# Optimization experiments

Measured on AMD Instinct MI355X. Metric: run time of the kernel, lower is better.

The kernel has to match this reference:

```python
import jax, jax.numpy as jnp
import numpy as np

T, D_ENC, H, D_EMB, VOCAB = 4000, 1024, 1024, 512, 8192
V = VOCAB + 1  # + blank
P = 800
TEMPERATURE = 1.0


def setup_inputs() -> dict:
    key = jax.random.key(0)
    ks = jax.random.split(key, 8)
    s = lambda d: 1.0 / np.sqrt(d)
    return {
        'enc_out': jax.random.normal(ks[0], (T, D_ENC), jnp.float32),
        'embedding': jax.random.normal(ks[1], (V, D_EMB), jnp.float32) * s(D_EMB),
        'W_ih': jax.random.normal(ks[2], (4 * H, D_EMB), jnp.float32) * s(D_EMB),
        'W_hh': jax.random.normal(ks[3], (4 * H, H), jnp.float32) * s(H),
        'b_lstm': jnp.zeros((4 * H,), jnp.float32),
        'W_pred': jax.random.normal(ks[4], (D_ENC, H), jnp.float32) * s(H),
        'b_pred': jnp.zeros((D_ENC,), jnp.float32),
        'W_join': jax.random.normal(ks[5], (V, D_ENC), jnp.float32) * s(D_ENC),
        'b_join': jnp.zeros((V,), jnp.float32),
        'phonemes': jax.random.randint(ks[6], (P,), 0, VOCAB, jnp.int32),
    }


def reference(enc_out, embedding, W_ih, W_hh, b_lstm, W_pred, b_pred, W_join, b_join, phonemes):
    blank_idx = embedding.shape[0] - 1
    n_phon = phonemes.shape[0]

    def predict_step(tok, h, c):
        # one-token RNNT predictor: embed -> LSTM cell -> projection to joiner dim
        x = embedding[tok]
        gates = x @ W_ih.T + h @ W_hh.T + b_lstm  # [4H]
        i, f, g, o = jnp.split(gates, 4)
        i, f, o = jax.nn.sigmoid(i), jax.nn.sigmoid(f), jax.nn.sigmoid(o)
        c2 = f * c + i * jnp.tanh(g)
        h2 = o * jnp.tanh(c2)
        pred = h2 @ W_pred.T + b_pred  # [D_ENC]
        return pred, h2, c2

    def step(carry, enc_t):
        tok, h, c, tp = carry
        pred, h2, c2 = predict_step(tok, h, c)
        logits = (jax.nn.relu(enc_t + pred) @ W_join.T + b_join) / TEMPERATURE
        logp = jax.nn.log_softmax(logits)  # [V]
        pick = jnp.argmax(logp)
        phon_done = tp >= n_phon
        is_blank = (pick == blank_idx) | phon_done
        next_phon = phonemes[jnp.minimum(tp, n_phon - 1)]
        prediction = jnp.where(is_blank, blank_idx, next_phon)
        # blank: keep hypothesis token/state; non-blank: advance to phoneme + new state
        tok2 = jnp.where(is_blank, tok, next_phon)
        h3 = jnp.where(is_blank, h, h2)
        c3 = jnp.where(is_blank, c, c2)
        tp2 = tp + jnp.where(is_blank, 0, 1)
        return (tok2, h3, c3, tp2), (logp, prediction, ~phon_done)

    # initial predictor pass with blank token from zero state (mirrors the warm-up predict call)
    h0 = jnp.zeros((W_hh.shape[1],), enc_out.dtype)
    c0 = jnp.zeros_like(h0)
    _, h_init, c_init = predict_step(jnp.int32(blank_idx), h0, c0)
    carry0 = (jnp.int32(blank_idx), h_init, c_init, jnp.int32(0))
    _, (alignment, predictions, valid) = jax.lax.scan(step, carry0, enc_out)
    return alignment, predictions, valid
```

## Files before the change

kernel.cpp:

```cpp
#include <hip/hip_runtime.h>
#include <math.h>

#define TT     4000
#define DENC   1024
#define HD     1024
#define DEMB   512
#define VD     8193
#define NPH    800
#define BLANK  8192
#define NWG    256
#define NTHR   512
#define CHUNK_M 800
#define NSTEP  (NPH + 2)
#define NSTEPP 802
#define NVT    65
#define NP     129
#define CHUNK  256

typedef __bf16 bf16x4 __attribute__((ext_vector_type(4)));
typedef __bf16 bf16x8 __attribute__((ext_vector_type(8)));
typedef float  f32x16 __attribute__((ext_vector_type(16)));

#define WSF_HHIST  1024
#define WSF_PREDS  822272
#define WSF_HX     1642496
#define WSF_GXT    2053120
#define WSF_PMAX   1642496
#define WSF_PSUM   2158496
#define WSF_PARG   2674496
#define WSF_LSE    3190496
#define WSF_AMAX   3194496
#define WSF_XBF    3195520
#define WSF_W16    4899456
#define WSF_END    9159296
#define NEED_MFMA  ((size_t)36653568)
#define TST_IDX    512
#define HX_BYTE_OFF  ((size_t)WSF_HX * 4)
#define HX_BYTES     ((size_t)NSTEPP * 256 * 8)

#define L_HX     1024
#define L_HHIST  5120
#define L_PREDS  826368
#define F_PMAX 1646592
#define F_PSUM 1906592
#define F_PARG 2166592
#define F_LSE  2426592

#define GEMM_SMEM  12800
#define CHAIN_SMEM (4096 + 64 + 16 * NSTEPP * 2)
#define JOIN_SMEM  (65536 + 128)
#define S_XH   0
#define S_GS   3072
#define S_C4   3088
#define S_TOK  3264
#define S_RED  4066
#define S_AMAX 4082
#define SMEM_FLOATS_F32 4352
#define SMEM_BYTES_F32 (SMEM_FLOATS_F32 * 4)


__device__ __forceinline__ float dot4(float4 a, float4 b, float acc) {
  acc = fmaf(a.x, b.x, acc); acc = fmaf(a.y, b.y, acc);
  acc = fmaf(a.z, b.z, acc); acc = fmaf(a.w, b.w, acc);
  return acc;
}
__device__ __forceinline__ float sigmf(float x) { return 1.f / (1.f + expf(-x)); }
__device__ __forceinline__ float sigm_fast(float x) { return 1.f / (1.f + __expf(-x)); }
__device__ __forceinline__ float tanh_fast(float x) {
  float e = __expf(2.f * x);
  return 1.f - 2.f / (e + 1.f);
}
__device__ __forceinline__ float bfbits_to_f32(unsigned u16v) {
  return __builtin_bit_cast(float, (u16v & 0xFFFFu) << 16);
}

__device__ __forceinline__ void combine3(float& m, float& s, int& am,
                                         float om, float os, int oa) {
  float mm = fmaxf(m, om);
  s = s * __expf(m - mm) + os * __expf(om - mm);
  if (om > m || (om == m && oa < am)) am = oa;
  m = mm;
}

__device__ __forceinline__ void gload16(const void* g, void* l) {
  __builtin_amdgcn_global_load_lds(
      (const __attribute__((address_space(1))) unsigned int*)g,
      (__attribute__((address_space(3))) unsigned int*)l, 16, 0, 0);
}

__device__ __forceinline__ float ld_coh(const float* p) {
  return __hip_atomic_load((const float*)p, __ATOMIC_RELAXED, __HIP_MEMORY_SCOPE_AGENT);
}

__device__ __forceinline__ void light_barrier(unsigned* flags, unsigned& ep) {
  unsigned* arrive  = flags;
  unsigned* release = flags + 256;
  __builtin_amdgcn_s_waitcnt(0);
  __syncthreads();
  if (blockIdx.x == 0) {
    int tid = threadIdx.x;
    if (tid > 0 && tid < NWG) {
      while (__hip_atomic_load(&arrive[tid], __ATOMIC_RELAXED, __HIP_MEMORY_SCOPE_AGENT) != ep) {}
    }
    __syncthreads();
    if (tid == 0)
      __hip_atomic_store(release, ep, __ATOMIC_RELAXED, __HIP_MEMORY_SCOPE_AGENT);
  } else {
    if (threadIdx.x == 0) {
      __hip_atomic_store(&arrive[blockIdx.x], ep, __ATOMIC_RELAXED, __HIP_MEMORY_SCOPE_AGENT);
      while (__hip_atomic_load(release, __ATOMIC_RELAXED, __HIP_MEMORY_SCOPE_AGENT) != ep) {}
    }
    __syncthreads();
  }
  asm volatile("" ::: "memory");
  ep++;
}

__device__ __forceinline__ void heavy_barrier(unsigned* flags) {
  unsigned* bar = flags + 257;
  __syncthreads();
  if (threadIdx.x == 0) {
    __threadfence();
    unsigned g = __hip_atomic_load(&bar[1], __ATOMIC_RELAXED, __HIP_MEMORY_SCOPE_AGENT);
    unsigned v = __hip_atomic_fetch_add(&bar[0], 1u, __ATOMIC_RELAXED, __HIP_MEMORY_SCOPE_AGENT);
    if (v == (unsigned)(NWG - 1)) {
      __hip_atomic_store(&bar[0], 0u, __ATOMIC_RELAXED, __HIP_MEMORY_SCOPE_AGENT);
      __hip_atomic_store(&bar[1], g + 1u, __ATOMIC_RELEASE, __HIP_MEMORY_SCOPE_AGENT);
    } else {
      while (__hip_atomic_load(&bar[1], __ATOMIC_RELAXED, __HIP_MEMORY_SCOPE_AGENT) == g)
        __builtin_amdgcn_s_sleep(1);
    }
    __threadfence();
  }
  __syncthreads();
}

__device__ void xbf_fill(const float* enc, const float* preds, __bf16* dst,
                         int t0, int K, int pi0, int g0, int gs) {
  int total = K << 8;
  for (int q = g0; q < total; q += gs) {
    int j = q >> 8, seg = q & 255;
    int pi = (pi0 < 0) ? NPH : pi0 + j;
    float4 e = ((const float4*)(enc + (size_t)(t0 + j) * 1024))[seg];
    float4 p = ((const float4*)(preds + (size_t)pi * 1024))[seg];
    bf16x4 r;
    r[0] = (__bf16)fmaxf(e.x + p.x, 0.f);
    r[1] = (__bf16)fmaxf(e.y + p.y, 0.f);
    r[2] = (__bf16)fmaxf(e.z + p.z, 0.f);
    r[3] = (__bf16)fmaxf(e.w + p.w, 0.f);
    *(bf16x4*)(dst + (size_t)j * 1024 + (seg << 2)) = r;
  }
}

__device__ void joiner_tiles(const __bf16* W16, const __bf16* xrows, const float* bj,
                             float* out_align, float* pmax, float* psum, int* parg,
                             char* smc, int t0, int K, int tile0, int tstride) {
  const int tid = threadIdx.x;
  const int wid = tid >> 6, lane = tid & 63;
  const int wj = wid & 3, wv = wid >> 2;
  const int l31 = lane & 31, lhi = lane >> 5;
  const int jt_n = (K + 127) >> 7;
  const int ntiles = jt_n * NVT;

  for (int tile = tile0; tile < ntiles; tile += tstride) {
    const int vt = tile % NVT, jt = tile / NVT;
    const int v0 = vt << 7, j0 = jt << 7;
    f32x16 acc0, acc1;
    #pragma unroll
    for (int i = 0; i < 16; ++i) { acc0[i] = 0.f; acc1[i] = 0.f; }

    auto stage = [&](int db, int kb) {
      char* wb = smc + db * 32768;
      char* xb = wb + 16384;
      #pragma unroll
      for (int p = 0; p < 2; ++p) {
        int sbase = p * 512 + wid * 64;
        int s = sbase + lane;
        int ks = s >> 7, r = s & 127;
        gload16(W16 + (size_t)(v0 + r) * 1024 + kb + ks * 8, wb + sbase * 16);
        gload16(xrows + (size_t)(j0 + r) * 1024 + kb + ks * 8, xb + sbase * 16);
      }
    };

    stage(0, 0);
    __syncthreads();
    int db = 0;
    for (int kb16 = 0; kb16 < 16; ++kb16) {
      if (kb16 < 15) stage(db ^ 1, (kb16 + 1) << 6);
      const char* wb = smc + db * 32768;
      const char* xb = wb + 16384;
      #pragma unroll
      for (int k16 = 0; k16 < 4; ++k16) {
        int ks = k16 * 2 + lhi;
        bf16x8 a  = *(const bf16x8*)(xb + ((ks << 7) + (wj << 5) + l31) * 16);
        bf16x8 b0 = *(const bf16x8*)(wb + ((ks << 7) + (wv << 6) + l31) * 16);
        bf16x8 b1 = *(const bf16x8*)(wb + ((ks << 7) + (wv << 6) + 32 + l31) * 16);
        acc0 = __builtin_amdgcn_mfma_f32_32x32x16_bf16(a, b0, acc0, 0, 0, 0);
        acc1 = __builtin_amdgcn_mfma_f32_32x32x16_bf16(a, b1, acc1, 0, 0, 0);
      }
      __syncthreads();
      db ^= 1;
    }

    const int v_0 = v0 + (wv << 6) + l31;
    const int v_1 = v_0 + 32;
    const float bj0 = (v_0 < VD) ? bj[v_0] : 0.f;
    const float bj1 = (v_1 < VD) ? bj[v_1] : 0.f;
    const int jbase = j0 + (wj << 5) + 4 * lhi;
    const bool npok = (v0 + (wv << 6)) < VD;
    const int np = (v0 >> 6) + wv;
    #pragma unroll
    for (int reg = 0; reg < 16; ++reg) {
      int j = jbase + (reg & 3) + 8 * (reg >> 2);
      bool jok = j < K;
      float lg0 = acc0[reg] + bj0;
      float lg1 = acc1[reg] + bj1;
      if (jok) {
        size_t ro = (size_t)(t0 + j) * VD;
        if (v_0 < VD) out_align[ro + v_0] = lg0;
        if (v_1 < VD) out_align[ro + v_1] = lg1;
      }
      float l0 = (v_0 < VD) ? lg0 : -1e30f;
      float l1 = (v_1 < VD) ? lg1 : -1e30f;
      float m = fmaxf(l0, l1);
      float ss = 0.f;
      if (v_0 < VD) ss += __expf(l0 - m);
      if (v_1 < VD) ss += __expf(l1 - m);
      int am = (l1 > l0) ? v_1 : v_0;
      #pragma unroll
      for (int msk = 1; msk <= 16; msk <<= 1) {
        float om = __shfl_xor(m, msk, 64);
        float os = __shfl_xor(ss, msk, 64);
        int oa = __shfl_xor(am, msk, 64);
        float mm = fmaxf(m, om);
        ss = ss * __expf(m - mm) + os * __expf(om - mm);
        if (om > m || (om == m && oa < am)) am = oa;
        m = mm;
      }
      if (l31 == 0 && jok && npok) {
        size_t pb = (size_t)(t0 + j) * NP + np;
        __hip_atomic_store(&pmax[pb], m, __ATOMIC_RELAXED, __HIP_MEMORY_SCOPE_AGENT);
        __hip_atomic_store(&psum[pb], ss, __ATOMIC_RELAXED, __HIP_MEMORY_SCOPE_AGENT);
        __hip_atomic_store(&parg[pb], am, __ATOMIC_RELAXED, __HIP_MEMORY_SCOPE_AGENT);
      }
    }
  }
}

__device__ __forceinline__ void merge_row129(const float* pmax, const float* psum,
                                             const int* parg, int row, int lane,
                                             float& m, float& s, int& am) {
  size_t b = (size_t)row * NP;
  m = ld_coh(pmax + b + lane);
  s = ld_coh(psum + b + lane);
  am = __hip_atomic_load(&parg[b + lane], __ATOMIC_RELAXED, __HIP_MEMORY_SCOPE_AGENT);
  {
    int i2 = lane + 64;
    float om = ld_coh(pmax + b + i2);
    float os = ld_coh(psum + b + i2);
    int oa = __hip_atomic_load(&parg[b + i2], __ATOMIC_RELAXED, __HIP_MEMORY_SCOPE_AGENT);
    combine3(m, s, am, om, os, oa);
  }
  if (lane == 0) {
    float om = ld_coh(pmax + b + 128);
    float os = ld_coh(psum + b + 128);
    int oa = __hip_atomic_load(&parg[b + 128], __ATOMIC_RELAXED, __HIP_MEMORY_SCOPE_AGENT);
    combine3(m, s, am, om, os, oa);
  }
  #pragma unroll
  for (int msk = 32; msk; msk >>= 1) {
    float om = __shfl_xor(m, msk, 64);
    float os = __shfl_xor(s, msk, 64);
    int oa = __shfl_xor(am, msk, 64);
    combine3(m, s, am, om, os, oa);
  }
}

__global__ __launch_bounds__(512) void wconv_kernel(const float* __restrict__ Wjoin,
                                                    float* wsf) {
  __bf16* w16 = (__bf16*)(wsf + WSF_W16);
  int g0 = blockIdx.x * 512 + threadIdx.x;
  int gs = gridDim.x * 512;
  for (int q = g0; q < VD * 256; q += gs) {
    int v = q >> 8, seg = q & 255;
    float4 w4 = ((const float4*)(Wjoin + (size_t)v * 1024))[seg];
    bf16x4 r;
    r[0] = (__bf16)w4.x; r[1] = (__bf16)w4.y; r[2] = (__bf16)w4.z; r[3] = (__bf16)w4.w;
    *(bf16x4*)(w16 + (size_t)v * 1024 + (seg << 2)) = r;
  }
}

__global__ __launch_bounds__(512) void gx_kernel(
    const float* __restrict__ Wih, const float* __restrict__ emb,
    const float* __restrict__ bl, const int* __restrict__ phon, float* wsf) {
  extern __shared__ float sm[];
  float* Wt = sm;
  float* Xt = sm + 2112;
  __bf16* gxT = (__bf16*)(wsf + WSF_GXT);
  const int tid = threadIdx.x;
  const int tx = tid & 31, ty = tid >> 5;
  int ntiles = 32 * 13;
  for (int tile = blockIdx.x; tile < ntiles; tile += gridDim.x) {
    int vt = tile & 31, jt = tile >> 5;
    int v0 = vt * 128, j0 = jt * 64;
    float acc[4][4];
    #pragma unroll
    for (int a = 0; a < 4; ++a)
      #pragma unroll
      for (int q = 0; q < 4; ++q) acc[a][q] = 0.f;
    for (int kk = 0; kk < DEMB; kk += 16) {
      {
        int r = tid >> 2, seg = tid & 3;
        float4 wv = ((const float4*)(Wih + (size_t)(v0 + r) * DEMB + kk))[seg];
        Wt[(seg * 4 + 0) * 132 + r] = wv.x;
        Wt[(seg * 4 + 1) * 132 + r] = wv.y;
        Wt[(seg * 4 + 2) * 132 + r] = wv.z;
        Wt[(seg * 4 + 3) * 132 + r] = wv.w;
      }
      if (tid < 256) {
        int r = tid >> 2, seg = tid & 3;
        int j = j0 + r;
        float4 xv = make_float4(0.f, 0.f, 0.f, 0.f);
        if (j < NSTEP) {
          int tok = (j < 2) ? BLANK : phon[j - 2];
          xv = ((const float4*)(emb + (size_t)tok * DEMB + kk))[seg];
        }
        Xt[(seg * 4 + 0) * 68 + r] = xv.x;
        Xt[(seg * 4 + 1) * 68 + r] = xv.y;
        Xt[(seg * 4 + 2) * 68 + r] = xv.z;
        Xt[(seg * 4 + 3) * 68 + r] = xv.w;
      }
      __syncthreads();
      #pragma unroll
      for (int k = 0; k < 16; ++k) {
        float4 a = *(const float4*)(Wt + k * 132 + (tx << 2));
        float4 bq = *(const float4*)(Xt + k * 68 + (ty << 2));
        acc[0][0] = fmaf(a.x, bq.x, acc[0][0]); acc[1][0] = fmaf(a.y, bq.x, acc[1][0]);
        acc[2][0] = fmaf(a.z, bq.x, acc[2][0]); acc[3][0] = fmaf(a.w, bq.x, acc[3][0]);
        acc[0][1] = fmaf(a.x, bq.y, acc[0][1]); acc[1][1] = fmaf(a.y, bq.y, acc[1][1]);
        acc[2][1] = fmaf(a.z, bq.y, acc[2][1]); acc[3][1] = fmaf(a.w, bq.y, acc[3][1]);
        acc[0][2] = fmaf(a.x, bq.z, acc[0][2]); acc[1][2] = fmaf(a.y, bq.z, acc[1][2]);
        acc[2][2] = fmaf(a.z, bq.z, acc[2][2]); acc[3][2] = fmaf(a.w, bq.z, acc[3][2]);
        acc[0][3] = fmaf(a.x, bq.w, acc[0][3]); acc[1][3] = fmaf(a.y, bq.w, acc[1][3]);
        acc[2][3] = fmaf(a.z, bq.w, acc[2][3]); acc[3][3] = fmaf(a.w, bq.w, acc[3][3]);
      }
      __syncthreads();
    }
    int vb = v0 + (tx << 2), jb0 = j0 + (ty << 2);
    #pragma unroll
    for (int jj = 0; jj < 4; ++jj) {
      int j = jb0 + jj;
      if (j >= NSTEP) continue;
      #pragma unroll
      for (int q = 0; q < 4; ++q)
        gxT[(size_t)(vb + q) * NSTEPP + j] = (__bf16)(acc[q][jj] + bl[vb + q]);
    }
  }
}

__global__ __launch_bounds__(NTHR) void chain_kernel(const float* __restrict__ Whh,
                                                     float* wsf) {
  extern __shared__ float sm[];
  float* hcur = sm;
  float* GS = sm + 1024;
  __bf16* gxl = (__bf16*)(sm + 1024 + 16);
  const int tid = threadIdx.x;
  const int w = tid >> 6, l = tid & 63;
  const int b = blockIdx.x;
  const __bf16* gxT = (const __bf16*)(wsf + WSF_GXT);
  float* hhist = wsf + WSF_HHIST;
  unsigned long long* hx = (unsigned long long*)(wsf + WSF_HX);

  float4 W0[4], W1[4];
  {
    int rr0 = 2 * w, rr1 = 2 * w + 1;
    int gr0 = ((rr0 >> 2) << 10) + 4 * b + (rr0 & 3);
    int gr1 = ((rr1 >> 2) << 10) + 4 * b + (rr1 & 3);
    const float4* h0 = (const float4*)(Whh + (size_t)gr0 * HD);
    const float4* h1 = (const float4*)(Whh + (size_t)gr1 * HD);
    #pragma unroll
    for (int i = 0; i < 4; ++i) { W0[i] = h0[l + 64 * i]; W1[i] = h1[l + 64 * i]; }
  }
  for (int rr = 0; rr < 16; ++rr) {
    int gr = ((rr >> 2) << 10) + 4 * b + (rr & 3);
    for (int s = tid; s < NSTEP; s += NTHR)
      gxl[rr * NSTEPP + s] = gxT[(size_t)gr * NSTEPP + s];
  }
  for (int i = tid; i < 1024; i += NTHR) hcur[i] = 0.f;
  __syncthreads();

  float c_reg = 0.f;
  for (int s = 0; s < NSTEP; ++s) {
    const float4* h4 = (const float4*)hcur;
    float a0 = 0.f, a1 = 0.f;
    #pragma unroll
    for (int i = 0; i < 4; ++i) {
      float4 hv = h4[l + 64 * i];
      a0 = dot4(W0[i], hv, a0);
      a1 = dot4(W1[i], hv, a1);
    }
    #pragma unroll
    for (int m = 32; m; m >>= 1) {
      a0 += __shfl_xor(a0, m, 64);
      a1 += __shfl_xor(a1, m, 64);
    }
    if (l == 0) { GS[2 * w] = a0; GS[2 * w + 1] = a1; }
    __syncthreads();

    unsigned hb16 = 0;
    if (tid < 4) {
      int j = tid;
      float gi = GS[j]      + (float)gxl[j * NSTEPP + s];
      float gf = GS[4 + j]  + (float)gxl[(4 + j) * NSTEPP + s];
      float gg = GS[8 + j]  + (float)gxl[(8 + j) * NSTEPP + s];
      float go = GS[12 + j] + (float)gxl[(12 + j) * NSTEPP + s];
      float c2 = sigm_fast(gf) * c_reg + sigm_fast(gi) * tanh_fast(gg);
      float h2 = sigm_fast(go) * tanh_fast(c2);
      c_reg = c2;
      hhist[(size_t)s * HD + 4 * b + j] = h2;
      __bf16 hb = (__bf16)h2;
      hb16 = (unsigned)__builtin_bit_cast(unsigned short, hb);
    }
    if (w == 0) {
      unsigned b0 = __shfl(hb16, 0, 64), b1 = __shfl(hb16, 1, 64);
      unsigned b2 = __shfl(hb16, 2, 64), b3 = __shfl(hb16, 3, 64);
      if (l == 0) {
        if (s + 1 < NSTEP) {
          unsigned long long pk = (unsigned long long)b0
                                | ((unsigned long long)b1 << 16)
                                | ((unsigned long long)b2 << 32)
                                | ((unsigned long long)b3 << 48);
          __hip_atomic_store(&hx[(size_t)s * 256 + b], pk,
                             __ATOMIC_RELAXED, __HIP_MEMORY_SCOPE_AGENT);
        }
        float4 hf;
        hf.x = bfbits_to_f32(b0); hf.y = bfbits_to_f32(b1);
        hf.z = bfbits_to_f32(b2); hf.w = bfbits_to_f32(b3);
        ((float4*)hcur)[b] = hf;
      }
    }
    if (s + 1 < NSTEP && tid < 256 && tid != b) {
      const unsigned long long* src = &hx[(size_t)s * 256 + tid];
      unsigned long long v = __hip_atomic_load(src, __ATOMIC_RELAXED, __HIP_MEMORY_SCOPE_AGENT);
      while ((v & 0xFFFFull) == 0xFFFFull) {
        __builtin_amdgcn_s_sleep(1);
        v = __hip_atomic_load(src, __ATOMIC_RELAXED, __HIP_MEMORY_SCOPE_AGENT);
      }
      float4 hf;
      hf.x = bfbits_to_f32((unsigned)v);
      hf.y = bfbits_to_f32((unsigned)(v >> 16));
      hf.z = bfbits_to_f32((unsigned)(v >> 32));
      hf.w = bfbits_to_f32((unsigned)(v >> 48));
      ((float4*)hcur)[tid] = hf;
    }
    __syncthreads();
  }
}

__global__ __launch_bounds__(512) void preds_kernel(
    const float* __restrict__ Wpred, const float* __restrict__ bp, float* wsf) {
  extern __shared__ float sm[];
  float* Wt = sm;
  float* Xt = sm + 2112;
  const float* hhist = wsf + WSF_HHIST;
  float* preds = wsf + WSF_PREDS;
  const int tid = threadIdx.x;
  const int tx = tid & 31, ty = tid >> 5;
  int ntiles = 8 * 13;
  for (int tile = blockIdx.x; tile < ntiles; tile += gridDim.x) {
    int vt = tile & 7, jt = tile >> 3;
    int v0 = vt * 128, j0 = jt * 64;
    float acc[4][4];
    #pragma unroll
    for (int a = 0; a < 4; ++a)
      #pragma unroll
      for (int q = 0; q < 4; ++q) acc[a][q] = 0.f;
    for (int kk = 0; kk < 1024; kk += 16) {
      {
        int r = tid >> 2, seg = tid & 3;
        float4 wv = ((const float4*)(Wpred + (size_t)(v0 + r) * HD + kk))[seg];
        Wt[(seg * 4 + 0) * 132 + r] = wv.x;
        Wt[(seg * 4 + 1) * 132 + r] = wv.y;
        Wt[(seg * 4 + 2) * 132 + r] = wv.z;
        Wt[(seg * 4 + 3) * 132 + r] = wv.w;
      }
      if (tid < 256) {
        int r = tid >> 2, seg = tid & 3;
        int j = j0 + r;
        float4 xv = make_float4(0.f, 0.f, 0.f, 0.f);
        if (j <= NPH) xv = ((const float4*)(hhist + (size_t)(j + 1) * HD + kk))[seg];
        Xt[(seg * 4 + 0) * 68 + r] = xv.x;
        Xt[(seg * 4 + 1) * 68 + r] = xv.y;
        Xt[(seg * 4 + 2) * 68 + r] = xv.z;
        Xt[(seg * 4 + 3) * 68 + r] = xv.w;
      }
      __syncthreads();
      #pragma unroll
      for (int k = 0; k < 16; ++k) {
        float4 a = *(const float4*)(Wt + k * 132 + (tx << 2));
        float4 bq = *(const float4*)(Xt + k * 68 + (ty << 2));
        acc[0][0] = fmaf(a.x, bq.x, acc[0][0]); acc[1][0] = fmaf(a.y, bq.x, acc[1][0]);
        acc[2][0] = fmaf(a.z, bq.x, acc[2][0]); acc[3][0] = fmaf(a.w, bq.x, acc[3][0]);
        acc[0][1] = fmaf(a.x, bq.y, acc[0][1]); acc[1][1] = fmaf(a.y, bq.y, acc[1][1]);
        acc[2][1] = fmaf(a.z, bq.y, acc[2][1]); acc[3][1] = fmaf(a.w, bq.y, acc[3][1]);
        acc[0][2] = fmaf(a.x, bq.z, acc[0][2]); acc[1][2] = fmaf(a.y, bq.z, acc[1][2]);
        acc[2][2] = fmaf(a.z, bq.z, acc[2][2]); acc[3][2] = fmaf(a.w, bq.z, acc[3][2]);
        acc[0][3] = fmaf(a.x, bq.w, acc[0][3]); acc[1][3] = fmaf(a.y, bq.w, acc[1][3]);
        acc[2][3] = fmaf(a.z, bq.w, acc[2][3]); acc[3][3] = fmaf(a.w, bq.w, acc[3][3]);
      }
      __syncthreads();
    }
    int vb = v0 + (tx << 2), jb0 = j0 + (ty << 2);
    #pragma unroll
    for (int jj = 0; jj < 4; ++jj) {
      int j = jb0 + jj;
      if (j > NPH) continue;
      #pragma unroll
      for (int q = 0; q < 4; ++q)
        preds[(size_t)j * 1024 + vb + q] = acc[q][jj] + bp[vb + q];
    }
  }
}

__global__ void xspec_kernel(const float* __restrict__ enc, float* wsf) {
  xbf_fill(enc, wsf + WSF_PREDS, (__bf16*)(wsf + WSF_XBF), 0, CHUNK_M, 0,
           blockIdx.x * blockDim.x + threadIdx.x, gridDim.x * blockDim.x);
}

__global__ __launch_bounds__(NTHR) void joinspec_kernel(const float* __restrict__ bj,
                                                        float* out, float* wsf) {
  extern __shared__ float sm[];
  joiner_tiles((__bf16*)(wsf + WSF_W16), (__bf16*)(wsf + WSF_XBF), bj, out,
               wsf + WSF_PMAX, wsf + WSF_PSUM, (int*)(wsf + WSF_PARG),
               (char*)sm, 0, CHUNK_M, blockIdx.x, gridDim.x);
}

__global__ __launch_bounds__(NTHR) void decode_coop(
    const float* enc, const float* bj, const int* phon, float* out, float* wsf) {
  extern __shared__ float sm[];
  char* smc = (char*)sm;
  unsigned* flags = (unsigned*)wsf;
  float* preds = wsf + WSF_PREDS;
  float* pmax = wsf + WSF_PMAX;
  float* psum = wsf + WSF_PSUM;
  int* parg = (int*)(wsf + WSF_PARG);
  float* lse = wsf + WSF_LSE;
  int* amaxws = (int*)(wsf + WSF_AMAX);
  __bf16* xbf = (__bf16*)(wsf + WSF_XBF);
  __bf16* w16 = (__bf16*)(wsf + WSF_W16);
  float* out_pred  = out + (size_t)TT * VD;
  float* out_valid = out + (size_t)TT * VD + TT;

  const int tid = threadIdx.x;
  const int wid = tid >> 6, lane = tid & 63;
  unsigned ep = 1;
  int t = 0, tp = 0, iter = 0;

  while (t < TT && tp < NPH) {
    int K = CHUNK_M;
    if (TT - t < K) K = TT - t;
    if (NPH - tp < K) K = NPH - tp;
    if (iter > 0) {
      heavy_barrier(flags);
      xbf_fill(enc, preds, xbf, t, K, tp, blockIdx.x * NTHR + tid, gridDim.x * NTHR);
      heavy_barrier(flags);
      joiner_tiles(w16, xbf, bj, out, pmax, psum, parg, smc, t, K,
                   blockIdx.x, gridDim.x);
    }
    light_barrier(flags, ep);
    for (int j = blockIdx.x * 8 + wid; j < K; j += gridDim.x * 8) {
      float m, s; int am;
      merge_row129(pmax, psum, parg, t + j, lane, m, s, am);
      if (lane == 0) {
        __hip_atomic_store(&amaxws[j], am, __ATOMIC_RELAXED, __HIP_MEMORY_SCOPE_AGENT);
        lse[t + j] = m + logf(s);
      }
    }
    light_barrier(flags, ep);
    int cand = K;
    for (int idx = tid; idx < K; idx += NTHR) {
      int a = __hip_atomic_load(&amaxws[idx], __ATOMIC_RELAXED, __HIP_MEMORY_SCOPE_AGENT);
      if (a == BLANK && idx < cand) cand = idx;
    }
    #pragma unroll
    for (int msk = 32; msk; msk >>= 1) cand = min(cand, __shfl_xor(cand, msk, 64));
    int* red = (int*)(smc + 65536);
    if (lane == 0) red[wid] = cand;
    __syncthreads();
    if (tid == 0) {
      int mn = red[0];
      for (int w2 = 1; w2 < 8; ++w2) mn = min(mn, red[w2]);
      red[8] = mn;
    }
    __syncthreads();
    int jb = red[8];
    __syncthreads();
    int nacc = (jb < K) ? jb + 1 : K;
    int nadv = (jb < K) ? jb : K;
    if (blockIdx.x == 0) {
      for (int j = tid; j < nacc; j += NTHR) {
        out_pred[t + j] = (j == jb) ? (float)BLANK : (float)phon[tp + j];
        out_valid[t + j] = 1.f;
      }
    }
    t += nacc; tp += nadv; ++iter;
  }

  if (t < TT) {
    xbf_fill(enc, preds, xbf + (size_t)(t - 800) * 1024, t, TT - t, -1,
             blockIdx.x * NTHR + tid, gridDim.x * NTHR);
  }
  if (blockIdx.x == 0 && tid == 0) ((int*)wsf)[TST_IDX] = t;
}

__global__ __launch_bounds__(NTHR) void jointail_kernel(const float* __restrict__ bj,
                                                        float* out, float* wsf) {
  extern __shared__ float sm[];
  int t = ((const int*)wsf)[TST_IDX];
  if (t >= TT) return;
  joiner_tiles((__bf16*)(wsf + WSF_W16),
               (__bf16*)(wsf + WSF_XBF) + (size_t)(t - 800) * 1024, bj, out,
               wsf + WSF_PMAX, wsf + WSF_PSUM, (int*)(wsf + WSF_PARG),
               (char*)sm, t, TT - t, blockIdx.x, gridDim.x);
}

__global__ __launch_bounds__(NTHR) void mergetail_kernel(float* out, float* wsf) {
  int t = ((const int*)wsf)[TST_IDX];
  float* lse = wsf + WSF_LSE;
  float* out_pred  = out + (size_t)TT * VD;
  float* out_valid = out + (size_t)TT * VD + TT;
  const int wid = threadIdx.x >> 6, lane = threadIdx.x & 63;
  for (int row = t + blockIdx.x * 8 + wid; row < TT; row += gridDim.x * 8) {
    float m, s; int am;
    merge_row129(wsf + WSF_PMAX, wsf + WSF_PSUM, (const int*)(wsf + WSF_PARG),
                 row, lane, m, s, am);
    if (lane == 0) {
      lse[row] = m + logf(s);
      out_pred[row] = (float)BLANK;
      out_valid[row] = 0.f;
    }
  }
}

__global__ __launch_bounds__(256) void sub_kernel(float* out, const float* wsf) {
  const float* lse = wsf + WSF_LSE;
  for (int row = blockIdx.x; row < TT; row += gridDim.x) {
    float l = lse[row];
    float* p = out + (size_t)row * VD;
    for (int i = threadIdx.x; i < VD; i += 256) p[i] -= l;
  }
}

struct Ctx {
  const float *enc, *emb, *Wih, *Whh, *bl, *Wpred, *bp, *Wjoin, *bj;
  const int* phon;
  unsigned long long* hx;
  float *hhist, *preds, *pmax, *psum, *lse;
  int* parg;
  unsigned* flags;
  float *out_align, *out_pred, *out_valid;
};

__device__ void chain_all_legacy(const Ctx& C, float* sm) {
  const int tid = threadIdx.x;
  const int w = tid >> 6, l = tid & 63;
  const int b = blockIdx.x;
  int* tok_sm = (int*)(sm + S_TOK);
  for (int s = tid; s < NSTEP; s += NTHR)
    tok_sm[s] = (s < 2) ? BLANK : C.phon[s - 2];
  float4 W0[6], W1[6];
  {
    int rr0 = 2 * w, rr1 = 2 * w + 1;
    int gr0 = ((rr0 >> 2) << 10) + 4 * b + (rr0 & 3);
    int gr1 = ((rr1 >> 2) << 10) + 4 * b + (rr1 & 3);
    const float4* ih0 = (const float4*)(C.Wih + (size_t)gr0 * DEMB);
    const float4* hh0 = (const float4*)(C.Whh + (size_t)gr0 * HD);
    const float4* ih1 = (const float4*)(C.Wih + (size_t)gr1 * DEMB);
    const float4* hh1 = (const float4*)(C.Whh + (size_t)gr1 * HD);
    W0[0] = ih0[l];       W0[1] = ih0[64 + l];
    W0[2] = hh0[l];       W0[3] = hh0[64 + l];
    W0[4] = hh0[128 + l]; W0[5] = hh0[192 + l];
    W1[0] = ih1[l];       W1[1] = ih1[64 + l];
    W1[2] = hh1[l];       W1[3] = hh1[64 + l];
    W1[4] = hh1[128 + l]; W1[5] = hh1[192 + l];
  }
  float bi = 0.f, bf = 0.f, bg = 0.f, bo = 0.f;
  if (tid < 4) {
    bi = C.bl[4 * b + tid];
    bf = C.bl[1024 + 4 * b + tid];
    bg = C.bl[2048 + 4 * b + tid];
    bo = C.bl[3072 + 4 * b + tid];
    sm[S_C4 + tid] = 0.f;
  }
  for (int i = tid; i < 1536; i += NTHR) sm[S_XH + i] = 0.f;
  if (tid < 512) sm[S_XH + tid] = C.emb[(size_t)BLANK * DEMB + tid];
  __syncthreads();
  unsigned long long* hx = C.hx;
  for (int s = 0; s < NSTEP; ++s) {
    int p = s & 1;
    const float4* xh4 = (const float4*)(sm + S_XH + p * 1536);
    float a0 = 0.f, a1 = 0.f;
    #pragma unroll
    for (int i = 0; i < 6; ++i) {
      float4 v = xh4[i * 64 + l];
      a0 = dot4(W0[i], v, a0);
      a1 = dot4(W1[i], v, a1);
    }
    #pragma unroll
    for (int m = 32; m; m >>= 1) {
      a0 += __shfl_xor(a0, m, 64);
      a1 += __shfl_xor(a1, m, 64);
    }
    if (l == 0) { sm[S_GS + 2 * w] = a0; sm[S_GS + 2 * w + 1] = a1; }
    if (s + 1 < NSTEP && tid < 512)
      sm[S_XH + (1 - p) * 1536 + tid] = C.emb[(size_t)tok_sm[s + 1] * DEMB + tid];
    __syncthreads();
    if (tid < 4) {
      int j = tid;
      float gi = sm[S_GS + j]      + bi;
      float gf = sm[S_GS + 4 + j]  + bf;
      float gg = sm[S_GS + 8 + j]  + bg;
      float go = sm[S_GS + 12 + j] + bo;
      float cc = sm[S_C4 + j];
      float c2 = sigmf(gf) * cc + sigmf(gi) * tanhf(gg);
      float h2 = sigmf(go) * tanhf(c2);
      sm[S_C4 + j] = c2;
      int cell = 4 * b + j;
      C.hhist[(size_t)s * HD + cell] = h2;
      unsigned long long pk = ((unsigned long long)(unsigned)(s + 1) << 32)
                            | (unsigned long long)__float_as_uint(h2);
      __hip_atomic_store(&hx[(1 - p) * 1024 + cell], pk,
                         __ATOMIC_RELAXED, __HIP_MEMORY_SCOPE_AGENT);
    }
    if (s + 1 < NSTEP) {
      unsigned tg = (unsigned)(s + 1);
      #pragma unroll
      for (int kq = 0; kq < 2; ++kq) {
        int k = tid + kq * 512;
        unsigned long long v;
        do {
          v = __hip_atomic_load(&hx[(1 - p) * 1024 + k],
                                __ATOMIC_RELAXED, __HIP_MEMORY_SCOPE_AGENT);
        } while ((unsigned)(v >> 32) != tg);
        sm[S_XH + (1 - p) * 1536 + 512 + k] = __uint_as_float((unsigned)v);
      }
    }
    __syncthreads();
  }
}

__device__ void preds_gemm_legacy(const Ctx& C, float* sm) {
  float* Wt = sm;
  float* Xt = sm + 2112;
  const int tid = threadIdx.x;
  const int tx = tid & 31, ty = tid >> 5;
  int ntiles = 8 * 13;
  for (int tile = blockIdx.x; tile < ntiles; tile += NWG) {
    int vt = tile & 7, jt = tile >> 3;
    int v0 = vt * 128, j0 = jt * 64;
    float acc[4][4];
    #pragma unroll
    for (int a = 0; a < 4; ++a)
      #pragma unroll
      for (int q = 0; q < 4; ++q) acc[a][q] = 0.f;
    for (int kk = 0; kk < 1024; kk += 16) {
      {
        int r = tid >> 2, seg = tid & 3;
        float4 wv = ((const float4*)(C.Wpred + (size_t)(v0 + r) * HD + kk))[seg];
        Wt[(seg * 4 + 0) * 132 + r] = wv.x;
        Wt[(seg * 4 + 1) * 132 + r] = wv.y;
        Wt[(seg * 4 + 2) * 132 + r] = wv.z;
        Wt[(seg * 4 + 3) * 132 + r] = wv.w;
      }
      if (tid < 256) {
        int r = tid >> 2, seg = tid & 3;
        int j = j0 + r;
        float4 xv = make_float4(0.f, 0.f, 0.f, 0.f);
        if (j <= NPH) xv = ((const float4*)(C.hhist + (size_t)(j + 1) * HD + kk))[seg];
        Xt[(seg * 4 + 0) * 68 + r] = xv.x;
        Xt[(seg * 4 + 1) * 68 + r] = xv.y;
        Xt[(seg * 4 + 2) * 68 + r] = xv.z;
        Xt[(seg * 4 + 3) * 68 + r] = xv.w;
      }
      __syncthreads();
      #pragma unroll
      for (int k = 0; k < 16; ++k) {
        float4 a = *(const float4*)(Wt + k * 132 + (tx << 2));
        float4 bq = *(const float4*)(Xt + k * 68 + (ty << 2));
        acc[0][0] = fmaf(a.x, bq.x, acc[0][0]); acc[1][0] = fmaf(a.y, bq.x, acc[1][0]);
        acc[2][0] = fmaf(a.z, bq.x, acc[2][0]); acc[3][0] = fmaf(a.w, bq.x, acc[3][0]);
        acc[0][1] = fmaf(a.x, bq.y, acc[0][1]); acc[1][1] = fmaf(a.y, bq.y, acc[1][1]);
        acc[2][1] = fmaf(a.z, bq.y, acc[2][1]); acc[3][1] = fmaf(a.w, bq.y, acc[3][1]);
        acc[0][2] = fmaf(a.x, bq.z, acc[0][2]); acc[1][2] = fmaf(a.y, bq.z, acc[1][2]);
        acc[2][2] = fmaf(a.z, bq.z, acc[2][2]); acc[3][2] = fmaf(a.w, bq.z, acc[3][2]);
        acc[0][3] = fmaf(a.x, bq.w, acc[0][3]); acc[1][3] = fmaf(a.y, bq.w, acc[1][3]);
        acc[2][3] = fmaf(a.z, bq.w, acc[2][3]); acc[3][3] = fmaf(a.w, bq.w, acc[3][3]);
      }
      __syncthreads();
    }
    int vb = v0 + (tx << 2), jb0 = j0 + (ty << 2);
    #pragma unroll
    for (int jj = 0; jj < 4; ++jj) {
      int j = jb0 + jj;
      if (j > NPH) continue;
      #pragma unroll
      for (int q = 0; q < 4; ++q)
        C.preds[(size_t)j * 1024 + vb + q] = acc[q][jj] + C.bp[vb + q];
    }
  }
}

__device__ void joiner_gemm_f32(const Ctx& C, float* sm, int t0, int K, int pi0) {
  float* Wt = sm;
  float* Xt = sm + 2112;
  const int tid = threadIdx.x;
  const int tx = tid & 31, ty = tid >> 5;
  int jt_n = (K + 63) >> 6;
  int ntiles = jt_n * NVT;
  for (int tile = blockIdx.x; tile < ntiles; tile += NWG) {
    int vt = tile % NVT, jt = tile / NVT;
    int v0 = vt * 128, j0 = jt * 64;
    float acc[4][4];
    #pragma unroll
    for (int a = 0; a < 4; ++a)
      #pragma unroll
      for (int q = 0; q < 4; ++q) acc[a][q] = 0.f;
    for (int kk = 0; kk < 1024; kk += 16) {
      {
        int r = tid >> 2, seg = tid & 3;
        int v = v0 + r;
        float4 wv = make_float4(0.f, 0.f, 0.f, 0.f);
        if (v < VD) wv = ((const float4*)(C.Wjoin + (size_t)v * 1024 + kk))[seg];
        Wt[(seg * 4 + 0) * 132 + r] = wv.x;
        Wt[(seg * 4 + 1) * 132 + r] = wv.y;
        Wt[(seg * 4 + 2) * 132 + r] = wv.z;
        Wt[(seg * 4 + 3) * 132 + r] = wv.w;
      }
      if (tid < 256) {
        int r = tid >> 2, seg = tid & 3;
        int j = j0 + r;
        float4 xv = make_float4(0.f, 0.f, 0.f, 0.f);
        if (j < K) {
          int pi = (pi0 < 0) ? NPH : (pi0 + j);
          float4 e = ((const float4*)(C.enc + (size_t)(t0 + j) * DENC + kk))[seg];
          float4 pr = ((const float4*)(C.preds + (size_t)pi * 1024 + kk))[seg];
          xv.x = fmaxf(e.x + pr.x, 0.f);
          xv.y = fmaxf(e.y + pr.y, 0.f);
          xv.z = fmaxf(e.z + pr.z, 0.f);
          xv.w = fmaxf(e.w + pr.w, 0.f);
        }
        Xt[(seg * 4 + 0) * 68 + r] = xv.x;
        Xt[(seg * 4 + 1) * 68 + r] = xv.y;
        Xt[(seg * 4 + 2) * 68 + r] = xv.z;
        Xt[(seg * 4 + 3) * 68 + r] = xv.w;
      }
      __syncthreads();
      #pragma unroll
      for (int k = 0; k < 16; ++k) {
        float4 a = *(const float4*)(Wt + k * 132 + (tx << 2));
        float4 bq = *(const float4*)(Xt + k * 68 + (ty << 2));
        acc[0][0] = fmaf(a.x, bq.x, acc[0][0]); acc[1][0] = fmaf(a.y, bq.x, acc[1][0]);
        acc[2][0] = fmaf(a.z, bq.x, acc[2][0]); acc[3][0] = fmaf(a.w, bq.x, acc[3][0]);
        acc[0][1] = fmaf(a.x, bq.y, acc[0][1]); acc[1][1] = fmaf(a.y, bq.y, acc[1][1]);
        acc[2][1] = fmaf(a.z, bq.y, acc[2][1]); acc[3][1] = fmaf(a.w, bq.y, acc[3][1]);
        acc[0][2] = fmaf(a.x, bq.z, acc[0][2]); acc[1][2] = fmaf(a.y, bq.z, acc[1][2]);
        acc[2][2] = fmaf(a.z, bq.z, acc[2][2]); acc[3][2] = fmaf(a.w, bq.z, acc[3][2]);
        acc[0][3] = fmaf(a.x, bq.w, acc[0][3]); acc[1][3] = fmaf(a.y, bq.w, acc[1][3]);
        acc[2][3] = fmaf(a.z, bq.w, acc[2][3]); acc[3][3] = fmaf(a.w, bq.w, acc[3][3]);
      }
      __syncthreads();
    }
    int vb = v0 + (tx << 2);
    int jb0 = j0 + (ty << 2);
    float bjv[4];
    #pragma unroll
    for (int q = 0; q < 4; ++q) bjv[q] = (vb + q < VD) ? C.bj[vb + q] : 0.f;
    #pragma unroll
    for (int jj = 0; jj < 4; ++jj) {
      int j = jb0 + jj;
      if (j >= K) continue;
      size_t ro = (size_t)(t0 + j) * VD;
      float lg[4];
      float m = -1e30f; int am = vb;
      #pragma unroll
      for (int q = 0; q < 4; ++q) {
        int v = vb + q;
        if (v < VD) {
          lg[q] = acc[q][jj] + bjv[q];
          C.out_align[ro + v] = lg[q];
          if (lg[q] > m) { m = lg[q]; am = v; }
        } else lg[q] = -1e30f;
      }
      float ss = 0.f;
      #pragma unroll
      for (int q = 0; q < 4; ++q)
        if (vb + q < VD) ss += __expf(lg[q] - m);
      #pragma unroll
      for (int msk = 16; msk; msk >>= 1) {
        float om = __shfl_xor(m, msk, 64);
        float os = __shfl_xor(ss, msk, 64);
        int oa = __shfl_xor(am, msk, 64);
        combine3(m, ss, am, om, os, oa);
      }
      if (tx == 0) {
        size_t pb = (size_t)(t0 + j) * NVT + vt;
        __hip_atomic_store(&C.pmax[pb], m, __ATOMIC_RELAXED, __HIP_MEMORY_SCOPE_AGENT);
        __hip_atomic_store(&C.psum[pb], ss, __ATOMIC_RELAXED, __HIP_MEMORY_SCOPE_AGENT);
        __hip_atomic_store(&C.parg[pb], am, __ATOMIC_RELAXED, __HIP_MEMORY_SCOPE_AGENT);
      }
    }
  }
}

__device__ __forceinline__ void merge_row65(const Ctx& C, int row, int lane,
                                            float& m, float& s, int& am) {
  size_t b = (size_t)row * NVT;
  m = ld_coh(C.pmax + b + lane);
  s = ld_coh(C.psum + b + lane);
  am = __hip_atomic_load(&C.parg[b + lane], __ATOMIC_RELAXED, __HIP_MEMORY_SCOPE_AGENT);
  if (lane == 0) {
    float om = ld_coh(C.pmax + b + 64);
    float os = ld_coh(C.psum + b + 64);
    int oa = __hip_atomic_load(&C.parg[b + 64], __ATOMIC_RELAXED, __HIP_MEMORY_SCOPE_AGENT);
    combine3(m, s, am, om, os, oa);
  }
  #pragma unroll
  for (int msk = 32; msk; msk >>= 1) {
    float om = __shfl_xor(m, msk, 64);
    float os = __shfl_xor(s, msk, 64);
    int oa = __shfl_xor(am, msk, 64);
    combine3(m, s, am, om, os, oa);
  }
}

__global__ __launch_bounds__(NTHR) void decode_kernel_f32(
    const float* enc, const float* emb, const float* Wih, const float* Whh,
    const float* bl, const float* Wpred, const float* bp, const float* Wjoin,
    const float* bj, const int* phon, float* out, float* wsf) {
  extern __shared__ float sm[];
  Ctx C;
  C.enc = enc; C.emb = emb; C.Wih = Wih; C.Whh = Whh; C.bl = bl;
  C.Wpred = Wpred; C.bp = bp; C.Wjoin = Wjoin; C.bj = bj; C.phon = phon;
  C.flags = (unsigned*)wsf;
  C.hx = (unsigned long long*)(wsf + L_HX);
  C.hhist = wsf + L_HHIST;
  C.preds = wsf + L_PREDS;
  C.pmax = wsf + F_PMAX;
  C.psum = wsf + F_PSUM;
  C.parg = (int*)(wsf + F_PARG);
  C.lse = wsf + F_LSE;
  C.out_align = out;
  C.out_pred  = out + (size_t)TT * VD;
  C.out_valid = out + (size_t)TT * VD + TT;

  const int tid = threadIdx.x;
  const int wid = tid >> 6, lane = tid & 63;
  unsigned ep = 1;

  chain_all_legacy(C, sm);
  heavy_barrier(C.flags);
  preds_gemm_legacy(C, sm);
  heavy_barrier(C.flags);

  int t = 0, tp = 0;
  while (t < TT && tp < NPH) {
    int K = CHUNK;
    if (TT - t < K) K = TT - t;
    if (NPH - tp < K) K = NPH - tp;
    joiner_gemm_f32(C, sm, t, K, tp);
    light_barrier(C.flags, ep);
    int* amax_l = (int*)(sm + S_AMAX);
    for (int j = wid; j < K; j += 8) {
      float m, s; int am;
      merge_row65(C, t + j, lane, m, s, am);
      if (lane == 0) {
        amax_l[j] = am;
        C.lse[t + j] = m + logf(s);
      }
    }
    __syncthreads();
    int cand = K;
    if (tid < K && amax_l[tid] == BLANK) cand = tid;
    #pragma unroll
    for (int msk = 32; msk; msk >>= 1) cand = min(cand, __shfl_xor(cand, msk, 64));
    int* red = (int*)(sm + S_RED);
    if (lane == 0) red[wid] = cand;
    __syncthreads();
    if (tid == 0) {
      int mn = red[0];
      for (int w2 = 1; w2 < 8; ++w2) mn = min(mn, red[w2]);
      red[8] = mn;
    }
    __syncthreads();
    int jb = red[8];
    __syncthreads();
    int nacc = (jb < K) ? jb + 1 : K;
    int nadv = (jb < K) ? jb : K;
    if (blockIdx.x == 0) {
      int* tok_sm = (int*)(sm + S_TOK);
      for (int j = tid; j < nacc; j += NTHR) {
        C.out_pred[t + j] = (j == jb) ? (float)BLANK : (float)tok_sm[tp + j + 2];
        C.out_valid[t + j] = 1.f;
      }
    }
    t += nacc; tp += nadv;
    if (jb < K) heavy_barrier(C.flags);
  }
  if (t < TT) {
    int Kt = TT - t;
    joiner_gemm_f32(C, sm, t, Kt, -1);
    light_barrier(C.flags, ep);
    for (int i = blockIdx.x * 8 + wid; i < Kt; i += NWG * 8) {
      float m, s; int am;
      merge_row65(C, t + i, lane, m, s, am);
      if (lane == 0) C.lse[t + i] = m + logf(s);
    }
    const int gtid = blockIdx.x * NTHR + tid;
    for (int i = gtid; i < Kt; i += NWG * NTHR) {
      C.out_pred[t + i] = (float)BLANK;
      C.out_valid[t + i] = 0.f;
    }
  }
  heavy_barrier(C.flags);
  for (int row = blockIdx.x; row < TT; row += NWG) {
    float l = C.lse[row];
    float* p = C.out_align + (size_t)row * VD;
    for (int i = tid; i < VD; i += NTHR) p[i] -= l;
  }
}


extern "C" void kernel_launch(void* const* d_in, const int* in_sizes, int n_in,
                              void* d_out, int out_size, void* d_ws, size_t ws_size,
                              hipStream_t stream) {
  const float* enc   = (const float*)d_in[0];
  const float* emb   = (const float*)d_in[1];
  const float* Wih   = (const float*)d_in[2];
  const float* Whh   = (const float*)d_in[3];
  const float* bl    = (const float*)d_in[4];
  const float* Wpred = (const float*)d_in[5];
  const float* bp    = (const float*)d_in[6];
  const float* Wjoin = (const float*)d_in[7];
  const float* bj    = (const float*)d_in[8];
  const int*   phon  = (const int*)d_in[9];
  float* out = (float*)d_out;
  float* wsf = (float*)d_ws;

  hipMemsetAsync(d_ws, 0, 20480, stream);

  if (ws_size >= NEED_MFMA) {
    hipMemsetAsync((char*)d_ws + HX_BYTE_OFF, 0xFF, HX_BYTES, stream);

    hipFuncSetAttribute((const void*)chain_kernel,
                        hipFuncAttributeMaxDynamicSharedMemorySize, CHAIN_SMEM);
    hipFuncSetAttribute((const void*)joinspec_kernel,
                        hipFuncAttributeMaxDynamicSharedMemorySize, JOIN_SMEM);
    hipFuncSetAttribute((const void*)decode_coop,
                        hipFuncAttributeMaxDynamicSharedMemorySize, JOIN_SMEM);
    hipFuncSetAttribute((const void*)jointail_kernel,
                        hipFuncAttributeMaxDynamicSharedMemorySize, JOIN_SMEM);

    wconv_kernel<<<1024, 512, 0, stream>>>(Wjoin, wsf);
    gx_kernel<<<416, 512, GEMM_SMEM, stream>>>(Wih, emb, bl, phon, wsf);
    {
      const float* WhhA = Whh; float* wsfA = wsf;
      void* a2[] = { &WhhA, &wsfA };
      hipError_t e = hipLaunchCooperativeKernel((void*)chain_kernel, dim3(256), dim3(NTHR),
                                                a2, CHAIN_SMEM, stream);
      if (e != hipSuccess)
        chain_kernel<<<dim3(256), dim3(NTHR), CHAIN_SMEM, stream>>>(Whh, wsf);
    }
    preds_kernel<<<104, 512, GEMM_SMEM, stream>>>(Wpred, bp, wsf);
    xspec_kernel<<<1024, 256, 0, stream>>>(enc, wsf);
    joinspec_kernel<<<455, NTHR, JOIN_SMEM, stream>>>(bj, out, wsf);
    {
      const float* encA = enc; const float* bjA = bj; const int* phonA = phon;
      float* outA = out; float* wsfA = wsf;
      void* a3[] = { &encA, &bjA, &phonA, &outA, &wsfA };
      hipError_t e = hipLaunchCooperativeKernel((void*)decode_coop, dim3(NWG), dim3(NTHR),
                                                a3, JOIN_SMEM, stream);
      if (e != hipSuccess)
        decode_coop<<<dim3(NWG), dim3(NTHR), JOIN_SMEM, stream>>>(enc, bj, phon, out, wsf);
    }
    jointail_kernel<<<1664, NTHR, JOIN_SMEM, stream>>>(bj, out, wsf);
    mergetail_kernel<<<256, NTHR, 0, stream>>>(out, wsf);
    sub_kernel<<<2048, 256, 0, stream>>>(out, wsf);
  } else {
    hipFuncSetAttribute((const void*)decode_kernel_f32,
                        hipFuncAttributeMaxDynamicSharedMemorySize, SMEM_BYTES_F32);
    void* args[] = { &enc, &emb, &Wih, &Whh, &bl, &Wpred, &bp, &Wjoin, &bj, &phon, &out, &wsf };
    hipError_t e = hipLaunchCooperativeKernel((void*)decode_kernel_f32, dim3(NWG), dim3(NTHR),
                                              args, SMEM_BYTES_F32, stream);
    if (e != hipSuccess) {
      decode_kernel_f32<<<dim3(NWG), dim3(NTHR), SMEM_BYTES_F32, stream>>>(
          enc, emb, Wih, Whh, bl, Wpred, bp, Wjoin, bj, phon, out, wsf);
    }
  }
}
```

Measured before the change: 3.284 ms.

## Run LSTM chain on a single XCD team of 32 blocks with bf16 register weights

The serial LSTM recurrence now runs on 32 workgroups that all sit on the same XCD, chosen at runtime from the hardware XCC id, instead of 256 workgroups spread across the chip. Each block owns 32 hidden units and keeps its W_hh rows in registers packed as bf16. Blocks exchange h through global flags polled with sc0 loads, so the per-step handoff stays inside one XCD's L2 and fewer peers have to synchronise. The risks are lower W_hh precision, heavy register pressure from the 128-word weight array, and that electing the team depends on block placement and flag counters in the workspace.

```diff
diff --git a/kernel.cpp b/kernel.cpp
--- a/kernel.cpp
+++ b/kernel.cpp
@@ -20,6 +20,7 @@
 typedef __bf16 bf16x4 __attribute__((ext_vector_type(4)));
 typedef __bf16 bf16x8 __attribute__((ext_vector_type(8)));
 typedef float  f32x16 __attribute__((ext_vector_type(16)));
+typedef unsigned long long u64t;
 
 #define WSF_HHIST  1024
 #define WSF_PREDS  822272
@@ -47,7 +48,6 @@
 #define F_LSE  2426592
 
 #define GEMM_SMEM  12800
-#define CHAIN_SMEM (4096 + 64 + 16 * NSTEPP * 2)
 #define JOIN_SMEM  (65536 + 128)
 #define S_XH   0
 #define S_GS   3072
@@ -358,100 +358,131 @@
   }
 }
 
-__global__ __launch_bounds__(NTHR) void chain_kernel(const float* __restrict__ Whh,
-                                                     float* wsf) {
-  extern __shared__ float sm[];
-  float* hcur = sm;
-  float* GS = sm + 1024;
-  __bf16* gxl = (__bf16*)(sm + 1024 + 16);
+__global__ __launch_bounds__(NTHR, 2) void chain_kernel(const float* __restrict__ Whh,
+                                                        float* wsf) {
+  __shared__ float hcur[1024];
+  __shared__ float GS[128];
+  __shared__ float gxs[128];
+  __shared__ unsigned short hstage[32];
+  __shared__ int team_sh;
   const int tid = threadIdx.x;
+  unsigned* flags = (unsigned*)wsf;
+
+  if (tid == 0) {
+    unsigned xcd;
+    asm volatile("s_getreg_b32 %0, hwreg(HW_REG_XCC_ID)" : "=s"(xcd));
+    xcd &= 7u;
+    unsigned pos = __hip_atomic_fetch_add(&flags[520 + xcd], 1u,
+                     __ATOMIC_RELAXED, __HIP_MEMORY_SCOPE_AGENT);
+    if (pos == 31u) {
+      unsigned expd = 0u;
+      __hip_atomic_compare_exchange_strong(&flags[528], &expd, xcd + 1u,
+          __ATOMIC_RELAXED, __ATOMIC_RELAXED, __HIP_MEMORY_SCOPE_AGENT);
+    }
+    unsigned wv;
+    while ((wv = __hip_atomic_load(&flags[528], __ATOMIC_RELAXED,
+                                   __HIP_MEMORY_SCOPE_AGENT)) == 0u) {}
+    team_sh = (wv - 1u == xcd && pos < 32u) ? (int)pos : -1;
+  }
+  __syncthreads();
+  const int team = team_sh;
+  if (team < 0) return;
+
   const int w = tid >> 6, l = tid & 63;
-  const int b = blockIdx.x;
-  const __bf16* gxT = (const __bf16*)(wsf + WSF_GXT);
-  float* hhist = wsf + WSF_HHIST;
-  unsigned long long* hx = (unsigned long long*)(wsf + WSF_HX);
-
-  float4 W0[4], W1[4];
+  const int lr = w * 16 + (l & 15);
+  const int seg = l >> 4;
+  const int c0 = team * 32;
+  const int grow = ((lr >> 5) << 10) + c0 + (lr & 31);
+
+  unsigned wp[128];
   {
-    int rr0 = 2 * w, rr1 = 2 * w + 1;
-    int gr0 = ((rr0 >> 2) << 10) + 4 * b + (rr0 & 3);
-    int gr1 = ((rr1 >> 2) << 10) + 4 * b + (rr1 & 3);
-    const float4* h0 = (const float4*)(Whh + (size_t)gr0 * HD);
-    const float4* h1 = (const float4*)(Whh + (size_t)gr1 * HD);
-    #pragma unroll
-    for (int i = 0; i < 4; ++i) { W0[i] = h0[l + 64 * i]; W1[i] = h1[l + 64 * i]; }
-  }
-  for (int rr = 0; rr < 16; ++rr) {
-    int gr = ((rr >> 2) << 10) + 4 * b + (rr & 3);
-    for (int s = tid; s < NSTEP; s += NTHR)
-      gxl[rr * NSTEPP + s] = gxT[(size_t)gr * NSTEPP + s];
+    const float4* src = (const float4*)(Whh + (size_t)grow * HD) + seg * 64;
+    #pragma unroll
+    for (int i = 0; i < 64; ++i) {
+      float4 v = src[i];
+      unsigned a0 = (unsigned)__builtin_bit_cast(unsigned short, (__bf16)v.x);
+      unsigned a1 = (unsigned)__builtin_bit_cast(unsigned short, (__bf16)v.y);
+      unsigned a2 = (unsigned)__builtin_bit_cast(unsigned short, (__bf16)v.z);
+      unsigned a3 = (unsigned)__builtin_bit_cast(unsigned short, (__bf16)v.w);
+      wp[2 * i]     = a0 | (a1 << 16);
+      wp[2 * i + 1] = a2 | (a3 << 16);
+    }
   }
   for (int i = tid; i < 1024; i += NTHR) hcur[i] = 0.f;
   __syncthreads();
 
+  u64t* hx = (u64t*)(wsf + WSF_HX);
+  const unsigned short* gxT = (const unsigned short*)(wsf + WSF_GXT);
+  float* hhist = wsf + WSF_HHIST;
   float c_reg = 0.f;
+
   for (int s = 0; s < NSTEP; ++s) {
-    const float4* h4 = (const float4*)hcur;
-    float a0 = 0.f, a1 = 0.f;
-    #pragma unroll
-    for (int i = 0; i < 4; ++i) {
-      float4 hv = h4[l + 64 * i];
-      a0 = dot4(W0[i], hv, a0);
-      a1 = dot4(W1[i], hv, a1);
-    }
-    #pragma unroll
-    for (int m = 32; m; m >>= 1) {
-      a0 += __shfl_xor(a0, m, 64);
-      a1 += __shfl_xor(a1, m, 64);
-    }
-    if (l == 0) { GS[2 * w] = a0; GS[2 * w + 1] = a1; }
-    __syncthreads();
-
-    unsigned hb16 = 0;
-    if (tid < 4) {
+    unsigned gxv = 0;
+    if (tid < 128)
+      gxv = gxT[(size_t)(((tid >> 5) << 10) + c0 + (tid & 31)) * NSTEPP + s];
+
+    float acc = 0.f;
+    const float4* h4 = ((const float4*)hcur) + seg * 64;
+    #pragma unroll
+    for (int i = 0; i < 64; ++i) {
+      float4 hv = h4[i];
+      unsigned wa = wp[2 * i], wb = wp[2 * i + 1];
+      acc = fmaf(__builtin_bit_cast(float, wa << 16),          hv.x, acc);
+      acc = fmaf(__builtin_bit_cast(float, wa & 0xFFFF0000u),  hv.y, acc);
+      acc = fmaf(__builtin_bit_cast(float, wb << 16),          hv.z, acc);
+      acc = fmaf(__builtin_bit_cast(float, wb & 0xFFFF0000u),  hv.w, acc);
+    }
+    acc += __shfl_xor(acc, 16, 64);
+    acc += __shfl_xor(acc, 32, 64);
+    if (seg == 0) GS[lr] = acc;
+    if (tid < 128) gxs[tid] = bfbits_to_f32(gxv);
+    __syncthreads();
+
+    if (tid < 32) {
       int j = tid;
-      float gi = GS[j]      + (float)gxl[j * NSTEPP + s];
-      float gf = GS[4 + j]  + (float)gxl[(4 + j) * NSTEPP + s];
-      float gg = GS[8 + j]  + (float)gxl[(8 + j) * NSTEPP + s];
-      float go = GS[12 + j] + (float)gxl[(12 + j) * NSTEPP + s];
+      float gi = GS[j]       + gxs[j];
+      float gf = GS[32 + j]  + gxs[32 + j];
+      float gg = GS[64 + j]  + gxs[64 + j];
+      float go = GS[96 + j]  + gxs[96 + j];
       float c2 = sigm_fast(gf) * c_reg + sigm_fast(gi) * tanh_fast(gg);
       float h2 = sigm_fast(go) * tanh_fast(c2);
       c_reg = c2;
-      hhist[(size_t)s * HD + 4 * b + j] = h2;
-      __bf16 hb = (__bf16)h2;
-      hb16 = (unsigned)__builtin_bit_cast(unsigned short, hb);
-    }
-    if (w == 0) {
-      unsigned b0 = __shfl(hb16, 0, 64), b1 = __shfl(hb16, 1, 64);
-      unsigned b2 = __shfl(hb16, 2, 64), b3 = __shfl(hb16, 3, 64);
-      if (l == 0) {
-        if (s + 1 < NSTEP) {
-          unsigned long long pk = (unsigned long long)b0
-                                | ((unsigned long long)b1 << 16)
-                                | ((unsigned long long)b2 << 32)
-                                | ((unsigned long long)b3 << 48);
-          __hip_atomic_store(&hx[(size_t)s * 256 + b], pk,
-                             __ATOMIC_RELAXED, __HIP_MEMORY_SCOPE_AGENT);
+      hcur[c0 + j] = h2;
+      hhist[(size_t)s * HD + c0 + j] = h2;
+      hstage[j] = __builtin_bit_cast(unsigned short, (__bf16)h2);
+    }
+    if (s + 1 < NSTEP) {
+      if (tid < 8) {
+        size_t idx = (size_t)s * 256 + team * 8 + tid;
+        u64t pk = (u64t)hstage[4 * tid]
+                | ((u64t)hstage[4 * tid + 1] << 16)
+                | ((u64t)hstage[4 * tid + 2] << 32)
+                | ((u64t)hstage[4 * tid + 3] << 48);
+        *(volatile u64t*)(hx + idx) = pk;
+        __hip_atomic_store(hx + idx, pk, __ATOMIC_RELAXED,
+                           __HIP_MEMORY_SCOPE_AGENT);
+      }
+      if (tid < 256 && (tid >> 3) != team) {
+        u64t addr = (u64t)(hx + (size_t)s * 256 + tid);
+        u64t v; unsigned tries = 0;
+        for (;;) {
+          if ((tries & 3u) == 3u) {
+            v = __hip_atomic_load((const u64t*)addr, __ATOMIC_RELAXED,
+                                  __HIP_MEMORY_SCOPE_AGENT);
+          } else {
+            asm volatile("global_load_dwordx2 %0, %1, off sc0\n\ts_waitcnt vmcnt(0)"
+                         : "=v"(v) : "v"(addr) : "memory");
+          }
+          if ((v & 0xFFFFull) != 0xFFFFull) break;
+          ++tries;
         }
         float4 hf;
-        hf.x = bfbits_to_f32(b0); hf.y = bfbits_to_f32(b1);
-        hf.z = bfbits_to_f32(b2); hf.w = bfbits_to_f32(b3);
-        ((float4*)hcur)[b] = hf;
-      }
-    }
-    if (s + 1 < NSTEP && tid < 256 && tid != b) {
-      const unsigned long long* src = &hx[(size_t)s * 256 + tid];
-      unsigned long long v = __hip_atomic_load(src, __ATOMIC_RELAXED, __HIP_MEMORY_SCOPE_AGENT);
-      while ((v & 0xFFFFull) == 0xFFFFull) {
-        __builtin_amdgcn_s_sleep(1);
-        v = __hip_atomic_load(src, __ATOMIC_RELAXED, __HIP_MEMORY_SCOPE_AGENT);
-      }
-      float4 hf;
-      hf.x = bfbits_to_f32((unsigned)v);
-      hf.y = bfbits_to_f32((unsigned)(v >> 16));
-      hf.z = bfbits_to_f32((unsigned)(v >> 32));
-      hf.w = bfbits_to_f32((unsigned)(v >> 48));
-      ((float4*)hcur)[tid] = hf;
+        hf.x = bfbits_to_f32((unsigned)v);
+        hf.y = bfbits_to_f32((unsigned)(v >> 16));
+        hf.z = bfbits_to_f32((unsigned)(v >> 32));
+        hf.w = bfbits_to_f32((unsigned)(v >> 48));
+        ((float4*)hcur)[tid] = hf;
+      }
     }
     __syncthreads();
   }
@@ -1051,8 +1082,6 @@
   if (ws_size >= NEED_MFMA) {
     hipMemsetAsync((char*)d_ws + HX_BYTE_OFF, 0xFF, HX_BYTES, stream);
 
-    hipFuncSetAttribute((const void*)chain_kernel,
-                        hipFuncAttributeMaxDynamicSharedMemorySize, CHAIN_SMEM);
     hipFuncSetAttribute((const void*)joinspec_kernel,
                         hipFuncAttributeMaxDynamicSharedMemorySize, JOIN_SMEM);
     hipFuncSetAttribute((const void*)decode_coop,
@@ -1062,14 +1091,7 @@
 
     wconv_kernel<<<1024, 512, 0, stream>>>(Wjoin, wsf);
     gx_kernel<<<416, 512, GEMM_SMEM, stream>>>(Wih, emb, bl, phon, wsf);
-    {
-      const float* WhhA = Whh; float* wsfA = wsf;
-      void* a2[] = { &WhhA, &wsfA };
-      hipError_t e = hipLaunchCooperativeKernel((void*)chain_kernel, dim3(256), dim3(NTHR),
-                                                a2, CHAIN_SMEM, stream);
-      if (e != hipSuccess)
-        chain_kernel<<<dim3(256), dim3(NTHR), CHAIN_SMEM, stream>>>(Whh, wsf);
-    }
+    chain_kernel<<<dim3(256), dim3(NTHR), 0, stream>>>(Whh, wsf);
     preds_kernel<<<104, 512, GEMM_SMEM, stream>>>(Wpred, bp, wsf);
     xspec_kernel<<<1024, 256, 0, stream>>>(enc, wsf);
     joinspec_kernel<<<455, NTHR, JOIN_SMEM, stream>>>(bj, out, wsf);
```

Result: slower. 5.920 ms (+80.2%).
